# Optimization experiments

Hardware: AMD Instinct MI355X
Metric: run time of the kernel (lower is better)

The kernel has to match this reference:

```python
import jax, jax.numpy as jnp
import numpy as np

KEY_DIM = 64
DENSE_DIM = 128
B, N, M = 8, 2048, 256


def setup_inputs() -> dict:
    key = jax.random.key(0)
    ks = jax.random.split(key, 10)
    s_in = 1.0 / np.sqrt(M)
    s_k = 1.0 / np.sqrt(KEY_DIM)
    s_d = 1.0 / np.sqrt(DENSE_DIM)
    return {
        "x": jax.random.normal(ks[0], (B, N, M), dtype=jnp.float32),
        "Wq": jax.random.normal(ks[1], (M, KEY_DIM), dtype=jnp.float32) * s_in,
        "Wk": jax.random.normal(ks[2], (M, KEY_DIM), dtype=jnp.float32) * s_in,
        "Wv": jax.random.normal(ks[3], (M, KEY_DIM), dtype=jnp.float32) * s_in,
        "W1": jax.random.normal(ks[4], (KEY_DIM, DENSE_DIM), dtype=jnp.float32) * s_k,
        "b1": jnp.zeros((DENSE_DIM,), dtype=jnp.float32),
        "W2": jax.random.normal(ks[5], (DENSE_DIM, DENSE_DIM), dtype=jnp.float32) * s_d,
        "b2": jnp.zeros((DENSE_DIM,), dtype=jnp.float32),
        "W3": jax.random.normal(ks[6], (DENSE_DIM, DENSE_DIM), dtype=jnp.float32) * s_d,
        "b3": jnp.zeros((DENSE_DIM,), dtype=jnp.float32),
    }


def reference(x, Wq, Wk, Wv, W1, b1, W2, b2, W3, b3):
    scale = np.sqrt(KEY_DIM).astype(np.float32)
    q = jnp.einsum('bnm,mk->bnk', x, Wq)
    k = jnp.einsum('bnm,mk->bnk', x, Wk)
    v = jnp.einsum('bnm,mk->bnk', x, Wv)
    scores = jnp.einsum('bik,bjk->bij', q, k) / scale  # [B, N, N]
    weights = jax.nn.softmax(scores, axis=-1)
    z = jnp.einsum('bij,bjk->bik', weights, v)  # [B, N, key_dim]
    h = jax.nn.elu(z @ W1 + b1)
    h = jax.nn.elu(h @ W2 + b2)
    out = jax.nn.elu(h @ W3 + b3)
    return out
```

## Files before the change

kernel.cpp:

```cpp
#include <hip/hip_runtime.h>
#include <cstdint>
#include <cstddef>

#define B_ 8
#define N_ 2048
#define M_ 256
#define KD 64
#define DD 128
#define BN (B_ * N_)
#define KSPLIT 4
#define KT_PER (N_ / 64 / KSPLIT)

typedef __attribute__((ext_vector_type(8))) short s16x8;
typedef __attribute__((ext_vector_type(4))) float f32x4;
typedef __attribute__((ext_vector_type(4))) unsigned int u32x4;

__device__ __forceinline__ float elu_f(float x) {
    return x > 0.f ? x : (__expf(x) - 1.f);
}

__device__ __forceinline__ unsigned short f2bf(float f) {
    unsigned int u = __float_as_uint(f);
    u = (u + 0x7FFFu + ((u >> 16) & 1u)) >> 16;
    return (unsigned short)u;
// ... 51 lines not shown
        int id2 = id - 6144;
        if (id2 < 1024) {
            ct = id2 >> 7; c = (id2 >> 6) & 1; lane = id2 & 63;
            W = W1; ncol = DD; ph = pW1h; pl = pW1l;
            base = ((ct * 2 + c) * 64 + lane) * 8;
        } else if (id2 < 3072) {
            int id3 = id2 - 1024;
            ct = id3 >> 8; c = (id3 >> 6) & 3; lane = id3 & 63;
            W = W2; ncol = DD; ph = pW2h; pl = pW2l;
            base = ((ct * 4 + c) * 64 + lane) * 8;
        } else {
            int id3 = id2 - 3072;
            ct = id3 >> 8; c = (id3 >> 6) & 3; lane = id3 & 63;
            W = W3; ncol = DD; ph = pW3h; pl = pW3l;
            base = ((ct * 4 + c) * 64 + lane) * 8;
        }
    }
    const int col = ct * 16 + (lane & 15);
    const int kb = c * 32 + (lane >> 4) * 8;
    #pragma unroll
    for (int j = 0; j < 8; ++j) {
        float v = W[(size_t)(kb + j) * ncol + col];
        unsigned short h = f2bf(v);
        ph[base + j] = h;
        pl[base + j] = bflo(v, h);
    }
}

__global__ __launch_bounds__(256)
void qkv_kernel(const float* __restrict__ x,
                const unsigned short* __restrict__ pQh,
                unsigned short* __restrict__ qb, unsigned short* __restrict__ kb,
                unsigned short* __restrict__ vtb) {
    __shared__ unsigned short xh[16 * 264];
    __shared__ float dbuf[16 * 204];
    const int t = threadIdx.x;
    const int row0 = blockIdx.x * 16;

    for (int i = t; i < 1024; i += 256) {
        int rr = i >> 6, c4 = i & 63;
        float4 v = reinterpret_cast<const float4*>(x + (size_t)(row0 + rr) * M_)[c4];
        ushort4 o;
        o.x = f2bf(v.x); o.y = f2bf(v.y); o.z = f2bf(v.z); o.w = f2bf(v.w);
        *reinterpret_cast<ushort4*>(&xh[rr * 264 + c4 * 4]) = o;
    }
    __syncthreads();

    const int w = t >> 6, l = t & 63, g = l >> 4, r = l & 15;

    f32x4 acc0 = {0.f, 0.f, 0.f, 0.f};
    f32x4 acc1 = {0.f, 0.f, 0.f, 0.f};
    f32x4 acc2 = {0.f, 0.f, 0.f, 0.f};
    const int t0 = 3 * w, t1 = 3 * w + 1, t2 = 3 * w + 2;

    #pragma unroll
    for (int c = 0; c < 8; ++c) {
        const s16x8 af = *reinterpret_cast<const s16x8*>(&xh[r * 264 + c * 32 + g * 8]);
        const s16x8 b0 = *reinterpret_cast<const s16x8*>(pQh + ((t0 * 8 + c) * 64 + l) * 8);
        const s16x8 b1 = *reinterpret_cast<const s16x8*>(pQh + ((t1 * 8 + c) * 64 + l) * 8);
        const s16x8 b2 = *reinterpret_cast<const s16x8*>(pQh + ((t2 * 8 + c) * 64 + l) * 8);
        acc0 = __builtin_amdgcn_mfma_f32_16x16x32_bf16(af, b0, acc0, 0, 0, 0);
        acc1 = __builtin_amdgcn_mfma_f32_16x16x32_bf16(af, b1, acc1, 0, 0, 0);
        acc2 = __builtin_amdgcn_mfma_f32_16x16x32_bf16(af, b2, acc2, 0, 0, 0);
    }

    {
        const int c0 = (t0 >> 2) * 68 + (t0 & 3) * 16 + r;
        const int c1 = (t1 >> 2) * 68 + (t1 & 3) * 16 + r;
        const int c2 = (t2 >> 2) * 68 + (t2 & 3) * 16 + r;
        #pragma unroll
        for (int reg = 0; reg < 4; ++reg) {
            dbuf[(4 * g + reg) * 204 + c0] = acc0[reg];
            dbuf[(4 * g + reg) * 204 + c1] = acc1[reg];
            dbuf[(4 * g + reg) * 204 + c2] = acc2[reg];
        }
    }
    __syncthreads();

    const int b = row0 >> 11, n0 = row0 & 2047;
    if (t < 128) {
        const int mat = t >> 6, rr = (t >> 2) & 15, cq = t & 3;
        const float* src = &dbuf[rr * 204 + mat * 68 + cq * 16];
        float4 v0 = *reinterpret_cast<const float4*>(src);
        float4 v1 = *reinterpret_cast<const float4*>(src + 4);
        float4 v2 = *reinterpret_cast<const float4*>(src + 8);
        float4 v3 = *reinterpret_cast<const float4*>(src + 12);
        const float sc = (mat == 0) ? 0.125f : 1.0f;
        uint4 o0, o1;
        o0.x = bfpack2(v0.x * sc, v0.y * sc);
        o0.y = bfpack2(v0.z * sc, v0.w * sc);
        o0.z = bfpack2(v1.x * sc, v1.y * sc);
        o0.w = bfpack2(v1.z * sc, v1.w * sc);
        o1.x = bfpack2(v2.x * sc, v2.y * sc);
        o1.y = bfpack2(v2.z * sc, v2.w * sc);
        o1.z = bfpack2(v3.x * sc, v3.y * sc);
        o1.w = bfpack2(v3.z * sc, v3.w * sc);
        unsigned short* dst = (mat == 0 ? qb : kb) + (size_t)(row0 + rr) * KD + cq * 16;
        *reinterpret_cast<uint4*>(dst)     = o0;
        *reinterpret_cast<uint4*>(dst + 8) = o1;
    } else if (t < 192) {
        const int d = t & 63;
        unsigned short tmp[16];
        #pragma unroll
        for (int i = 0; i < 16; ++i)
            tmp[i] = f2bf(dbuf[i * 204 + 136 + d]);
        uint4 o0, o1;
        o0.x = (unsigned)tmp[0]  | ((unsigned)tmp[1]  << 16);
        o0.y = (unsigned)tmp[2]  | ((unsigned)tmp[3]  << 16);
        o0.z = (unsigned)tmp[4]  | ((unsigned)tmp[5]  << 16);
        o0.w = (unsigned)tmp[6]  | ((unsigned)tmp[7]  << 16);
        o1.x = (unsigned)tmp[8]  | ((unsigned)tmp[9]  << 16);
        o1.y = (unsigned)tmp[10] | ((unsigned)tmp[11] << 16);
        o1.z = (unsigned)tmp[12] | ((unsigned)tmp[13] << 16);
        o1.w = (unsigned)tmp[14] | ((unsigned)tmp[15] << 16);
        unsigned short* vp = vtb + ((size_t)b * KD + d) * N_ + n0;
        *reinterpret_cast<uint4*>(vp)     = o0;
        *reinterpret_cast<uint4*>(vp + 8) = o1;
    }
}

__global__ __launch_bounds__(256)
void attn_kernel(const unsigned short* __restrict__ qb,
                 const unsigned short* __restrict__ kb,
                 const unsigned short* __restrict__ vtb,
                 float* __restrict__ Zp, float* __restrict__ lsum) {
    __shared__ __align__(16) unsigned short ks[64 * 72];
    __shared__ __align__(16) unsigned short vt[64 * 72];
    __shared__ __align__(16) unsigned short ps[4 * 16 * 72];

    const int t = threadIdx.x;
    const int w = t >> 6;
    const int l = t & 63;
    const int g = l >> 4;
    const int r = l & 15;
    const int bid = blockIdx.x;
    const int split = bid & 3;
    const int qt = (bid >> 2) & 31;
    const int bb = bid >> 7;
    const int qrow0 = qt * 64 + w * 16;
    const int k0 = split * (N_ / KSPLIT);

    const unsigned short* qrow = qb + ((size_t)bb * N_ + qrow0 + r) * KD + g * 8;
    const s16x8 qf0 = *reinterpret_cast<const s16x8*>(qrow);
    const s16x8 qf1 = *reinterpret_cast<const s16x8*>(qrow + 32);

    const unsigned short* kbase = kb + ((size_t)bb * N_ + k0) * KD;
    const unsigned short* vbase = vtb + (size_t)bb * KD * N_ + k0;
    unsigned short* psw = ps + w * (16 * 72);

    for (int c = t; c < 512; c += 256) {
        int key = c >> 3, sub = c & 7;
        *reinterpret_cast<s16x8*>(&ks[key * 72 + sub * 8]) =
            *reinterpret_cast<const s16x8*>(kbase + (size_t)key * KD + sub * 8);
        *reinterpret_cast<s16x8*>(&vt[key * 72 + sub * 8]) =
            *reinterpret_cast<const s16x8*>(vbase + (size_t)key * N_ + sub * 8);
    }
    __syncthreads();

    f32x4 zac0 = {0.f, 0.f, 0.f, 0.f};
    f32x4 zac1 = {0.f, 0.f, 0.f, 0.f};
    f32x4 zac2 = {0.f, 0.f, 0.f, 0.f};
    f32x4 zac3 = {0.f, 0.f, 0.f, 0.f};
    float lacc[4] = {0.f, 0.f, 0.f, 0.f};

    const int ck0 = (t >> 3), cs0 = (t & 7);
    const int ck1 = ((t + 256) >> 3), cs1 = ((t + 256) & 7);

    for (int kt = 0; kt < KT_PER; ++kt) {
        s16x8 kr0, kr1, vr0, vr1;
        const bool pf = (kt + 1 < KT_PER);
        if (pf) {
            const unsigned short* kg = kbase + (size_t)(kt + 1) * 64 * KD;
            const unsigned short* vg = vbase + (size_t)(kt + 1) * 64;
            kr0 = *reinterpret_cast<const s16x8*>(kg + (size_t)ck0 * KD + cs0 * 8);
            kr1 = *reinterpret_cast<const s16x8*>(kg + (size_t)ck1 * KD + cs1 * 8);
            vr0 = *reinterpret_cast<const s16x8*>(vg + (size_t)ck0 * N_ + cs0 * 8);
            vr1 = *reinterpret_cast<const s16x8*>(vg + (size_t)ck1 * N_ + cs1 * 8);
        }

        f32x4 s0 = {0.f, 0.f, 0.f, 0.f};
        f32x4 s1 = {0.f, 0.f, 0.f, 0.f};
        f32x4 s2 = {0.f, 0.f, 0.f, 0.f};
        f32x4 s3 = {0.f, 0.f, 0.f, 0.f};
        {
            const s16x8 kf00 = *reinterpret_cast<const s16x8*>(&ks[(r +  0) * 72 + g * 8]);
            const s16x8 kf01 = *reinterpret_cast<const s16x8*>(&ks[(r +  0) * 72 + g * 8 + 32]);
            const s16x8 kf10 = *reinterpret_cast<const s16x8*>(&ks[(r + 16) * 72 + g * 8]);
            const s16x8 kf11 = *reinterpret_cast<const s16x8*>(&ks[(r + 16) * 72 + g * 8 + 32]);
            const s16x8 kf20 = *reinterpret_cast<const s16x8*>(&ks[(r + 32) * 72 + g * 8]);
            const s16x8 kf21 = *reinterpret_cast<const s16x8*>(&ks[(r + 32) * 72 + g * 8 + 32]);
            const s16x8 kf30 = *reinterpret_cast<const s16x8*>(&ks[(r + 48) * 72 + g * 8]);
            const s16x8 kf31 = *reinterpret_cast<const s16x8*>(&ks[(r + 48) * 72 + g * 8 + 32]);
            s0 = __builtin_amdgcn_mfma_f32_16x16x32_bf16(qf0, kf00, s0, 0, 0, 0);
            s0 = __builtin_amdgcn_mfma_f32_16x16x32_bf16(qf1, kf01, s0, 0, 0, 0);
            s1 = __builtin_amdgcn_mfma_f32_16x16x32_bf16(qf0, kf10, s1, 0, 0, 0);
            s1 = __builtin_amdgcn_mfma_f32_16x16x32_bf16(qf1, kf11, s1, 0, 0, 0);
            s2 = __builtin_amdgcn_mfma_f32_16x16x32_bf16(qf0, kf20, s2, 0, 0, 0);
            s2 = __builtin_amdgcn_mfma_f32_16x16x32_bf16(qf1, kf21, s2, 0, 0, 0);
            s3 = __builtin_amdgcn_mfma_f32_16x16x32_bf16(qf0, kf30, s3, 0, 0, 0);
            s3 = __builtin_amdgcn_mfma_f32_16x16x32_bf16(qf1, kf31, s3, 0, 0, 0);
        }

        const s16x8 vf00 = *reinterpret_cast<const s16x8*>(&vt[(r +  0) * 72 + g * 8]);
        const s16x8 vf01 = *reinterpret_cast<const s16x8*>(&vt[(r +  0) * 72 + g * 8 + 32]);
        const s16x8 vf10 = *reinterpret_cast<const s16x8*>(&vt[(r + 16) * 72 + g * 8]);
        const s16x8 vf11 = *reinterpret_cast<const s16x8*>(&vt[(r + 16) * 72 + g * 8 + 32]);
        const s16x8 vf20 = *reinterpret_cast<const s16x8*>(&vt[(r + 32) * 72 + g * 8]);
        const s16x8 vf21 = *reinterpret_cast<const s16x8*>(&vt[(r + 32) * 72 + g * 8 + 32]);
        const s16x8 vf30 = *reinterpret_cast<const s16x8*>(&vt[(r + 48) * 72 + g * 8]);
        const s16x8 vf31 = *reinterpret_cast<const s16x8*>(&vt[(r + 48) * 72 + g * 8 + 32]);

        #pragma unroll
        for (int j = 0; j < 4; ++j) {
            float p0 = __expf(s0[j]);
            float p1 = __expf(s1[j]);
            float p2 = __expf(s2[j]);
            float p3 = __expf(s3[j]);
            lacc[j] += (p0 + p1) + (p2 + p3);
            psw[(4 * g + j) * 72 + r +  0] = f2bf(p0);
            psw[(4 * g + j) * 72 + r + 16] = f2bf(p1);
            psw[(4 * g + j) * 72 + r + 32] = f2bf(p2);
            psw[(4 * g + j) * 72 + r + 48] = f2bf(p3);
        }

        asm volatile("s_waitcnt lgkmcnt(0)" ::: "memory");
        __builtin_amdgcn_sched_barrier(0);

        const s16x8 pa0 = *reinterpret_cast<const s16x8*>(&psw[r * 72 + g * 8]);
        const s16x8 pa1 = *reinterpret_cast<const s16x8*>(&psw[r * 72 + g * 8 + 32]);
        zac0 = __builtin_amdgcn_mfma_f32_16x16x32_bf16(pa0, vf00, zac0, 0, 0, 0);
        zac0 = __builtin_amdgcn_mfma_f32_16x16x32_bf16(pa1, vf01, zac0, 0, 0, 0);
        zac1 = __builtin_amdgcn_mfma_f32_16x16x32_bf16(pa0, vf10, zac1, 0, 0, 0);
        zac1 = __builtin_amdgcn_mfma_f32_16x16x32_bf16(pa1, vf11, zac1, 0, 0, 0);
        zac2 = __builtin_amdgcn_mfma_f32_16x16x32_bf16(pa0, vf20, zac2, 0, 0, 0);
        zac2 = __builtin_amdgcn_mfma_f32_16x16x32_bf16(pa1, vf21, zac2, 0, 0, 0);
        zac3 = __builtin_amdgcn_mfma_f32_16x16x32_bf16(pa0, vf30, zac3, 0, 0, 0);
        zac3 = __builtin_amdgcn_mfma_f32_16x16x32_bf16(pa1, vf31, zac3, 0, 0, 0);

        __syncthreads();
        if (pf) {
            *reinterpret_cast<s16x8*>(&ks[ck0 * 72 + cs0 * 8]) = kr0;
            *reinterpret_cast<s16x8*>(&ks[ck1 * 72 + cs1 * 8]) = kr1;
            *reinterpret_cast<s16x8*>(&vt[ck0 * 72 + cs0 * 8]) = vr0;
            *reinterpret_cast<s16x8*>(&vt[ck1 * 72 + cs1 * 8]) = vr1;
        }
        __syncthreads();
    }

    const size_t rowbase = (size_t)split * BN + (size_t)bb * N_ + qrow0;
    #pragma unroll
    for (int j = 0; j < 4; ++j) {
        float lt = lacc[j];
        lt += __shfl_xor(lt, 1);
        lt += __shfl_xor(lt, 2);
        lt += __shfl_xor(lt, 4);
        lt += __shfl_xor(lt, 8);
        if (r == 0)
            lsum[rowbase + 4 * g + j] = lt;
        float* zr = Zp + (rowbase + 4 * g + j) * KD + r;
        zr[ 0] = zac0[j];
        zr[16] = zac1[j];
        zr[32] = zac2[j];
        zr[48] = zac3[j];
    }
}

__global__ __launch_bounds__(256)
void mlp_kernel(const float* __restrict__ Zp, const float* __restrict__ lsum,
                const unsigned short* __restrict__ pW1h, const unsigned short* __restrict__ pW1l,
                const unsigned short* __restrict__ pW2h, const unsigned short* __restrict__ pW2l,
                const unsigned short* __restrict__ pW3h, const unsigned short* __restrict__ pW3l,
                const float* __restrict__ b1, const float* __restrict__ b2,
                const float* __restrict__ b3, float* __restrict__ out) {
    __shared__ unsigned int zW[16 * 68];
    __shared__ unsigned int hW[16 * 140];
    const int t = threadIdx.x;
    const int row0 = blockIdx.x * 16;

    {
        const int rr = t >> 4, dq = (t & 15) * 4;
        const size_t grow = (size_t)row0 + rr;
        const float inv = 1.0f / (lsum[grow] + lsum[BN + grow] +
                                  lsum[2 * (size_t)BN + grow] + lsum[3 * (size_t)BN + grow]);
        const size_t off = grow * KD + dq;
        float4 v0 = *reinterpret_cast<const float4*>(Zp + off);
        float4 v1 = *reinterpret_cast<const float4*>(Zp + (size_t)BN * KD + off);
        float4 v2 = *reinterpret_cast<const float4*>(Zp + 2 * (size_t)BN * KD + off);
        float4 v3 = *reinterpret_cast<const float4*>(Zp + 3 * (size_t)BN * KD + off);
        uint4 wv;
        wv.x = packw((v0.x + v1.x + v2.x + v3.x) * inv);
        wv.y = packw((v0.y + v1.y + v2.y + v3.y) * inv);
        wv.z = packw((v0.z + v1.z + v2.z + v3.z) * inv);
        wv.w = packw((v0.w + v1.w + v2.w + v3.w) * inv);
        *reinterpret_cast<uint4*>(&zW[rr * 68 + dq]) = wv;
    }
    __syncthreads();

    const int w = t >> 6, l = t & 63, g = l >> 4, r = l & 15;
    const int ctA = 2 * w, ctB = 2 * w + 1;

    f32x4 a1A = {0.f, 0.f, 0.f, 0.f};
    f32x4 a1B = {0.f, 0.f, 0.f, 0.f};
    #pragma unroll
    for (int c = 0; c < 2; ++c) {
        s16x8 ahi, alo;
        unpack8(&zW[r * 68 + c * 32 + g * 8], ahi, alo);
        const int baseA = ((ctA * 2 + c) * 64 + l) * 8;
        const int baseB = ((ctB * 2 + c) * 64 + l) * 8;
        const s16x8 bhA = *reinterpret_cast<const s16x8*>(pW1h + baseA);
        const s16x8 blA = *reinterpret_cast<const s16x8*>(pW1l + baseA);
        const s16x8 bhB = *reinterpret_cast<const s16x8*>(pW1h + baseB);
        const s16x8 blB = *reinterpret_cast<const s16x8*>(pW1l + baseB);
        a1A = __builtin_amdgcn_mfma_f32_16x16x32_bf16(ahi, bhA, a1A, 0, 0, 0);
        a1A = __builtin_amdgcn_mfma_f32_16x16x32_bf16(ahi, blA, a1A, 0, 0, 0);
        a1A = __builtin_amdgcn_mfma_f32_16x16x32_bf16(alo, bhA, a1A, 0, 0, 0);
        a1B = __builtin_amdgcn_mfma_f32_16x16x32_bf16(ahi, bhB, a1B, 0, 0, 0);
        a1B = __builtin_amdgcn_mfma_f32_16x16x32_bf16(ahi, blB, a1B, 0, 0, 0);
        a1B = __builtin_amdgcn_mfma_f32_16x16x32_bf16(alo, bhB, a1B, 0, 0, 0);
    }
    {
        const float bvA = b1[ctA * 16 + r], bvB = b1[ctB * 16 + r];
        #pragma unroll
        for (int reg = 0; reg < 4; ++reg) {
            hW[(4 * g + reg) * 140 + ctA * 16 + r] = packw(elu_f(a1A[reg] + bvA));
            hW[(4 * g + reg) * 140 + ctB * 16 + r] = packw(elu_f(a1B[reg] + bvB));
        }
    }
    __syncthreads();

    f32x4 a2A = {0.f, 0.f, 0.f, 0.f};
    f32x4 a2B = {0.f, 0.f, 0.f, 0.f};
    #pragma unroll
    for (int c = 0; c < 4; ++c) {
        s16x8 ahi, alo;
        unpack8(&hW[r * 140 + c * 32 + g * 8], ahi, alo);
        const int baseA = ((ctA * 4 + c) * 64 + l) * 8;
        const int baseB = ((ctB * 4 + c) * 64 + l) * 8;
        const s16x8 bhA = *reinterpret_cast<const s16x8*>(pW2h + baseA);
        const s16x8 blA = *reinterpret_cast<const s16x8*>(pW2l + baseA);
        const s16x8 bhB = *reinterpret_cast<const s16x8*>(pW2h + baseB);
        const s16x8 blB = *reinterpret_cast<const s16x8*>(pW2l + baseB);
        a2A = __builtin_amdgcn_mfma_f32_16x16x32_bf16(ahi, bhA, a2A, 0, 0, 0);
        a2A = __builtin_amdgcn_mfma_f32_16x16x32_bf16(ahi, blA, a2A, 0, 0, 0);
        a2A = __builtin_amdgcn_mfma_f32_16x16x32_bf16(alo, bhA, a2A, 0, 0, 0);
        a2B = __builtin_amdgcn_mfma_f32_16x16x32_bf16(ahi, bhB, a2B, 0, 0, 0);
        a2B = __builtin_amdgcn_mfma_f32_16x16x32_bf16(ahi, blB, a2B, 0, 0, 0);
        a2B = __builtin_amdgcn_mfma_f32_16x16x32_bf16(alo, bhB, a2B, 0, 0, 0);
    }
    __syncthreads();
    {
        const float bvA = b2[ctA * 16 + r], bvB = b2[ctB * 16 + r];
        #pragma unroll
        for (int reg = 0; reg < 4; ++reg) {
            hW[(4 * g + reg) * 140 + ctA * 16 + r] = packw(elu_f(a2A[reg] + bvA));
            hW[(4 * g + reg) * 140 + ctB * 16 + r] = packw(elu_f(a2B[reg] + bvB));
        }
    }
    __syncthreads();

    f32x4 a3A = {0.f, 0.f, 0.f, 0.f};
    f32x4 a3B = {0.f, 0.f, 0.f, 0.f};
    #pragma unroll
    for (int c = 0; c < 4; ++c) {
        s16x8 ahi, alo;
        unpack8(&hW[r * 140 + c * 32 + g * 8], ahi, alo);
        const int baseA = ((ctA * 4 + c) * 64 + l) * 8;
        const int baseB = ((ctB * 4 + c) * 64 + l) * 8;
        const s16x8 bhA = *reinterpret_cast<const s16x8*>(pW3h + baseA);
        const s16x8 blA = *reinterpret_cast<const s16x8*>(pW3l + baseA);
        const s16x8 bhB = *reinterpret_cast<const s16x8*>(pW3h + baseB);
        const s16x8 blB = *reinterpret_cast<const s16x8*>(pW3l + baseB);
        a3A = __builtin_amdgcn_mfma_f32_16x16x32_bf16(ahi, bhA, a3A, 0, 0, 0);
        a3A = __builtin_amdgcn_mfma_f32_16x16x32_bf16(ahi, blA, a3A, 0, 0, 0);
        a3A = __builtin_amdgcn_mfma_f32_16x16x32_bf16(alo, bhA, a3A, 0, 0, 0);
        a3B = __builtin_amdgcn_mfma_f32_16x16x32_bf16(ahi, bhB, a3B, 0, 0, 0);
        a3B = __builtin_amdgcn_mfma_f32_16x16x32_bf16(ahi, blB, a3B, 0, 0, 0);
        a3B = __builtin_amdgcn_mfma_f32_16x16x32_bf16(alo, bhB, a3B, 0, 0, 0);
    }
    {
        const float bvA = b3[ctA * 16 + r], bvB = b3[ctB * 16 + r];
        #pragma unroll
        for (int reg = 0; reg < 4; ++reg) {
            float* orow = out + (size_t)(row0 + 4 * g + reg) * DD;
            orow[ctA * 16 + r] = elu_f(a3A[reg] + bvA);
            orow[ctB * 16 + r] = elu_f(a3B[reg] + bvB);
        }
    }
}

extern "C" void kernel_launch(void* const* d_in, const int* in_sizes, int n_in,
                              void* d_out, int out_size, void* d_ws, size_t ws_size,
                              hipStream_t stream) {
    (void)in_sizes; (void)n_in; (void)out_size; (void)ws_size;
    const float* x  = (const float*)d_in[0];
    const float* Wq = (const float*)d_in[1];
    const float* Wk = (const float*)d_in[2];
    const float* Wv = (const float*)d_in[3];
    const float* W1 = (const float*)d_in[4];
    const float* b1 = (const float*)d_in[5];
    const float* W2 = (const float*)d_in[6];
    const float* b2 = (const float*)d_in[7];
    const float* W3 = (const float*)d_in[8];
    const float* b3 = (const float*)d_in[9];
    float* out = (float*)d_out;

    const size_t nt = (size_t)BN * KD;
    unsigned short* qbf = (unsigned short*)d_ws;
    unsigned short* kbf = qbf + nt;
    unsigned short* vtb = kbf + nt;
    float* Zp   = (float*)(vtb + nt);
    float* lsum = Zp + (size_t)KSPLIT * nt;
    unsigned short* pQh  = (unsigned short*)(lsum + (size_t)KSPLIT * BN);
    unsigned short* pQl  = pQh + 49152;
    unsigned short* pW1h = pQl + 49152;
    unsigned short* pW1l = pW1h + 8192;
    unsigned short* pW2h = pW1l + 8192;
    unsigned short* pW2l = pW2h + 16384;
    unsigned short* pW3h = pW2l + 16384;
    unsigned short* pW3l = pW3h + 16384;

    pack_kernel<<<dim3(44), 256, 0, stream>>>(Wq, Wk, Wv, W1, W2, W3,
                                              pQh, pQl, pW1h, pW1l, pW2h, pW2l, pW3h, pW3l);
    qkv_kernel<<<dim3(BN / 16), 256, 0, stream>>>(x, pQh, qbf, kbf, vtb);
    attn_kernel<<<dim3(BN / 64 * KSPLIT), 256, 0, stream>>>(qbf, kbf, vtb, Zp, lsum);
    mlp_kernel<<<dim3(BN / 16), 256, 0, stream>>>(Zp, lsum, pW1h, pW1l, pW2h, pW2l,
                                                  pW3h, pW3l, b1, b2, b3, out);
}
```

Baseline: 54.80 us.

## Give each wave two 16-row tiles in qkv, attention and MLP kernels

Each wave now handles 32 rows instead of 16 in all three main kernels. The qkv and MLP kernels process 32 rows per block, and attention uses 2 waves of 128 threads per block, each covering 32 query rows. The aim is to reuse the loaded B fragments (weights, K and V tiles) across two MFMA row tiles, halving fragment loads per flop and cutting global/LDS traffic per output. The cost is more registers per wave, fewer waves per block in attention, and half as many blocks in qkv and MLP, which lowers occupancy and parallelism.

```diff
diff --git a/kernel.cpp b/kernel.cpp
--- a/kernel.cpp
+++ b/kernel.cpp
@@ -107,12 +107,12 @@
                 const unsigned short* __restrict__ pQh,
                 unsigned short* __restrict__ qb, unsigned short* __restrict__ kb,
                 unsigned short* __restrict__ vtb) {
-    __shared__ unsigned short xh[16 * 264];
-    __shared__ float dbuf[16 * 204];
+    __shared__ unsigned short xh[32 * 264];
+    __shared__ float dbuf[32 * 204];
     const int t = threadIdx.x;
-    const int row0 = blockIdx.x * 16;
-
-    for (int i = t; i < 1024; i += 256) {
+    const int row0 = blockIdx.x * 32;
+
+    for (int i = t; i < 2048; i += 256) {
         int rr = i >> 6, c4 = i & 63;
         float4 v = reinterpret_cast<const float4*>(x + (size_t)(row0 + rr) * M_)[c4];
         ushort4 o;
@@ -122,21 +122,28 @@
     __syncthreads();
 
     const int w = t >> 6, l = t & 63, g = l >> 4, r = l & 15;
-
-    f32x4 acc0 = {0.f, 0.f, 0.f, 0.f};
-    f32x4 acc1 = {0.f, 0.f, 0.f, 0.f};
-    f32x4 acc2 = {0.f, 0.f, 0.f, 0.f};
     const int t0 = 3 * w, t1 = 3 * w + 1, t2 = 3 * w + 2;
 
+    f32x4 acc[3][2];
+    #pragma unroll
+    for (int m = 0; m < 3; ++m)
+        #pragma unroll
+        for (int s = 0; s < 2; ++s)
+            acc[m][s] = (f32x4){0.f, 0.f, 0.f, 0.f};
+
     #pragma unroll
     for (int c = 0; c < 8; ++c) {
-        const s16x8 af = *reinterpret_cast<const s16x8*>(&xh[r * 264 + c * 32 + g * 8]);
+        const s16x8 a0 = *reinterpret_cast<const s16x8*>(&xh[r * 264 + c * 32 + g * 8]);
+        const s16x8 a1 = *reinterpret_cast<const s16x8*>(&xh[(16 + r) * 264 + c * 32 + g * 8]);
         const s16x8 b0 = *reinterpret_cast<const s16x8*>(pQh + ((t0 * 8 + c) * 64 + l) * 8);
         const s16x8 b1 = *reinterpret_cast<const s16x8*>(pQh + ((t1 * 8 + c) * 64 + l) * 8);
         const s16x8 b2 = *reinterpret_cast<const s16x8*>(pQh + ((t2 * 8 + c) * 64 + l) * 8);
-        acc0 = __builtin_amdgcn_mfma_f32_16x16x32_bf16(af, b0, acc0, 0, 0, 0);
-        acc1 = __builtin_amdgcn_mfma_f32_16x16x32_bf16(af, b1, acc1, 0, 0, 0);
-        acc2 = __builtin_amdgcn_mfma_f32_16x16x32_bf16(af, b2, acc2, 0, 0, 0);
+        acc[0][0] = __builtin_amdgcn_mfma_f32_16x16x32_bf16(a0, b0, acc[0][0], 0, 0, 0);
+        acc[0][1] = __builtin_amdgcn_mfma_f32_16x16x32_bf16(a1, b0, acc[0][1], 0, 0, 0);
+        acc[1][0] = __builtin_amdgcn_mfma_f32_16x16x32_bf16(a0, b1, acc[1][0], 0, 0, 0);
+        acc[1][1] = __builtin_amdgcn_mfma_f32_16x16x32_bf16(a1, b1, acc[1][1], 0, 0, 0);
+        acc[2][0] = __builtin_amdgcn_mfma_f32_16x16x32_bf16(a0, b2, acc[2][0], 0, 0, 0);
+        acc[2][1] = __builtin_amdgcn_mfma_f32_16x16x32_bf16(a1, b2, acc[2][1], 0, 0, 0);
     }
 
     {
@@ -144,17 +151,20 @@
         const int c1 = (t1 >> 2) * 68 + (t1 & 3) * 16 + r;
         const int c2 = (t2 >> 2) * 68 + (t2 & 3) * 16 + r;
         #pragma unroll
-        for (int reg = 0; reg < 4; ++reg) {
-            dbuf[(4 * g + reg) * 204 + c0] = acc0[reg];
-            dbuf[(4 * g + reg) * 204 + c1] = acc1[reg];
-            dbuf[(4 * g + reg) * 204 + c2] = acc2[reg];
-        }
+        for (int s = 0; s < 2; ++s)
+            #pragma unroll
+            for (int reg = 0; reg < 4; ++reg) {
+                const int rw = (s * 16 + 4 * g + reg) * 204;
+                dbuf[rw + c0] = acc[0][s][reg];
+                dbuf[rw + c1] = acc[1][s][reg];
+                dbuf[rw + c2] = acc[2][s][reg];
+            }
     }
     __syncthreads();
 
     const int b = row0 >> 11, n0 = row0 & 2047;
-    if (t < 128) {
-        const int mat = t >> 6, rr = (t >> 2) & 15, cq = t & 3;
+    {
+        const int mat = t >> 7, rem = t & 127, rr = rem >> 2, cq = rem & 3;
         const float* src = &dbuf[rr * 204 + mat * 68 + cq * 16];
         float4 v0 = *reinterpret_cast<const float4*>(src);
         float4 v1 = *reinterpret_cast<const float4*>(src + 4);
@@ -173,35 +183,30 @@
         unsigned short* dst = (mat == 0 ? qb : kb) + (size_t)(row0 + rr) * KD + cq * 16;
         *reinterpret_cast<uint4*>(dst)     = o0;
         *reinterpret_cast<uint4*>(dst + 8) = o1;
-    } else if (t < 192) {
-        const int d = t & 63;
-        unsigned short tmp[16];
-        #pragma unroll
-        for (int i = 0; i < 16; ++i)
-            tmp[i] = f2bf(dbuf[i * 204 + 136 + d]);
-        uint4 o0, o1;
-        o0.x = (unsigned)tmp[0]  | ((unsigned)tmp[1]  << 16);
-        o0.y = (unsigned)tmp[2]  | ((unsigned)tmp[3]  << 16);
-        o0.z = (unsigned)tmp[4]  | ((unsigned)tmp[5]  << 16);
-        o0.w = (unsigned)tmp[6]  | ((unsigned)tmp[7]  << 16);
-        o1.x = (unsigned)tmp[8]  | ((unsigned)tmp[9]  << 16);
-        o1.y = (unsigned)tmp[10] | ((unsigned)tmp[11] << 16);
-        o1.z = (unsigned)tmp[12] | ((unsigned)tmp[13] << 16);
-        o1.w = (unsigned)tmp[14] | ((unsigned)tmp[15] << 16);
-        unsigned short* vp = vtb + ((size_t)b * KD + d) * N_ + n0;
-        *reinterpret_cast<uint4*>(vp)     = o0;
-        *reinterpret_cast<uint4*>(vp + 8) = o1;
-    }
-}
-
-__global__ __launch_bounds__(256)
+    }
+    {
+        const int d = t >> 2, ng = (t & 3) * 8;
+        unsigned short tmp[8];
+        #pragma unroll
+        for (int i = 0; i < 8; ++i)
+            tmp[i] = f2bf(dbuf[(ng + i) * 204 + 136 + d]);
+        uint4 o0;
+        o0.x = (unsigned)tmp[0] | ((unsigned)tmp[1] << 16);
+        o0.y = (unsigned)tmp[2] | ((unsigned)tmp[3] << 16);
+        o0.z = (unsigned)tmp[4] | ((unsigned)tmp[5] << 16);
+        o0.w = (unsigned)tmp[6] | ((unsigned)tmp[7] << 16);
+        *reinterpret_cast<uint4*>(vtb + ((size_t)b * KD + d) * N_ + n0 + ng) = o0;
+    }
+}
+
+__global__ __launch_bounds__(128)
 void attn_kernel(const unsigned short* __restrict__ qb,
                  const unsigned short* __restrict__ kb,
                  const unsigned short* __restrict__ vtb,
                  float* __restrict__ Zp, float* __restrict__ lsum) {
     __shared__ __align__(16) unsigned short ks[64 * 72];
     __shared__ __align__(16) unsigned short vt[64 * 72];
-    __shared__ __align__(16) unsigned short ps[4 * 16 * 72];
+    __shared__ __align__(16) unsigned short ps[2 * 32 * 72];
 
     const int t = threadIdx.x;
     const int w = t >> 6;
@@ -212,18 +217,21 @@
     const int split = bid & 3;
     const int qt = (bid >> 2) & 31;
     const int bb = bid >> 7;
-    const int qrow0 = qt * 64 + w * 16;
+    const int qrow0 = qt * 64 + w * 32;
     const int k0 = split * (N_ / KSPLIT);
 
-    const unsigned short* qrow = qb + ((size_t)bb * N_ + qrow0 + r) * KD + g * 8;
-    const s16x8 qf0 = *reinterpret_cast<const s16x8*>(qrow);
-    const s16x8 qf1 = *reinterpret_cast<const s16x8*>(qrow + 32);
+    const unsigned short* qrowA = qb + ((size_t)bb * N_ + qrow0 + r) * KD + g * 8;
+    const unsigned short* qrowB = qrowA + (size_t)16 * KD;
+    const s16x8 qfA0 = *reinterpret_cast<const s16x8*>(qrowA);
+    const s16x8 qfA1 = *reinterpret_cast<const s16x8*>(qrowA + 32);
+    const s16x8 qfB0 = *reinterpret_cast<const s16x8*>(qrowB);
+    const s16x8 qfB1 = *reinterpret_cast<const s16x8*>(qrowB + 32);
 
     const unsigned short* kbase = kb + ((size_t)bb * N_ + k0) * KD;
     const unsigned short* vbase = vtb + (size_t)bb * KD * N_ + k0;
-    unsigned short* psw = ps + w * (16 * 72);
-
-    for (int c = t; c < 512; c += 256) {
+    unsigned short* psw = ps + w * (32 * 72);
+
+    for (int c = t; c < 512; c += 128) {
         int key = c >> 3, sub = c & 7;
         *reinterpret_cast<s16x8*>(&ks[key * 72 + sub * 8]) =
             *reinterpret_cast<const s16x8*>(kbase + (size_t)key * KD + sub * 8);
@@ -232,31 +240,31 @@
     }
     __syncthreads();
 
-    f32x4 zac0 = {0.f, 0.f, 0.f, 0.f};
-    f32x4 zac1 = {0.f, 0.f, 0.f, 0.f};
-    f32x4 zac2 = {0.f, 0.f, 0.f, 0.f};
-    f32x4 zac3 = {0.f, 0.f, 0.f, 0.f};
-    float lacc[4] = {0.f, 0.f, 0.f, 0.f};
-
-    const int ck0 = (t >> 3), cs0 = (t & 7);
-    const int ck1 = ((t + 256) >> 3), cs1 = ((t + 256) & 7);
+    f32x4 zacA0 = {0.f,0.f,0.f,0.f}, zacA1 = {0.f,0.f,0.f,0.f};
+    f32x4 zacA2 = {0.f,0.f,0.f,0.f}, zacA3 = {0.f,0.f,0.f,0.f};
+    f32x4 zacB0 = {0.f,0.f,0.f,0.f}, zacB1 = {0.f,0.f,0.f,0.f};
+    f32x4 zacB2 = {0.f,0.f,0.f,0.f}, zacB3 = {0.f,0.f,0.f,0.f};
+    float laccA[4] = {0.f, 0.f, 0.f, 0.f};
+    float laccB[4] = {0.f, 0.f, 0.f, 0.f};
 
     for (int kt = 0; kt < KT_PER; ++kt) {
-        s16x8 kr0, kr1, vr0, vr1;
+        s16x8 kr[4], vr[4];
         const bool pf = (kt + 1 < KT_PER);
         if (pf) {
             const unsigned short* kg = kbase + (size_t)(kt + 1) * 64 * KD;
             const unsigned short* vg = vbase + (size_t)(kt + 1) * 64;
-            kr0 = *reinterpret_cast<const s16x8*>(kg + (size_t)ck0 * KD + cs0 * 8);
-            kr1 = *reinterpret_cast<const s16x8*>(kg + (size_t)ck1 * KD + cs1 * 8);
-            vr0 = *reinterpret_cast<const s16x8*>(vg + (size_t)ck0 * N_ + cs0 * 8);
-            vr1 = *reinterpret_cast<const s16x8*>(vg + (size_t)ck1 * N_ + cs1 * 8);
-        }
-
-        f32x4 s0 = {0.f, 0.f, 0.f, 0.f};
-        f32x4 s1 = {0.f, 0.f, 0.f, 0.f};
-        f32x4 s2 = {0.f, 0.f, 0.f, 0.f};
-        f32x4 s3 = {0.f, 0.f, 0.f, 0.f};
+            #pragma unroll
+            for (int i = 0; i < 4; ++i) {
+                const int c = t + 128 * i, key = c >> 3, sub = c & 7;
+                kr[i] = *reinterpret_cast<const s16x8*>(kg + (size_t)key * KD + sub * 8);
+                vr[i] = *reinterpret_cast<const s16x8*>(vg + (size_t)key * N_ + sub * 8);
+            }
+        }
+
+        f32x4 sA0 = {0.f,0.f,0.f,0.f}, sA1 = {0.f,0.f,0.f,0.f};
+        f32x4 sA2 = {0.f,0.f,0.f,0.f}, sA3 = {0.f,0.f,0.f,0.f};
+        f32x4 sB0 = {0.f,0.f,0.f,0.f}, sB1 = {0.f,0.f,0.f,0.f};
+        f32x4 sB2 = {0.f,0.f,0.f,0.f}, sB3 = {0.f,0.f,0.f,0.f};
         {
             const s16x8 kf00 = *reinterpret_cast<const s16x8*>(&ks[(r +  0) * 72 + g * 8]);
             const s16x8 kf01 = *reinterpret_cast<const s16x8*>(&ks[(r +  0) * 72 + g * 8 + 32]);
@@ -266,14 +274,22 @@
             const s16x8 kf21 = *reinterpret_cast<const s16x8*>(&ks[(r + 32) * 72 + g * 8 + 32]);
             const s16x8 kf30 = *reinterpret_cast<const s16x8*>(&ks[(r + 48) * 72 + g * 8]);
             const s16x8 kf31 = *reinterpret_cast<const s16x8*>(&ks[(r + 48) * 72 + g * 8 + 32]);
-            s0 = __builtin_amdgcn_mfma_f32_16x16x32_bf16(qf0, kf00, s0, 0, 0, 0);
-            s0 = __builtin_amdgcn_mfma_f32_16x16x32_bf16(qf1, kf01, s0, 0, 0, 0);
-            s1 = __builtin_amdgcn_mfma_f32_16x16x32_bf16(qf0, kf10, s1, 0, 0, 0);
-            s1 = __builtin_amdgcn_mfma_f32_16x16x32_bf16(qf1, kf11, s1, 0, 0, 0);
-            s2 = __builtin_amdgcn_mfma_f32_16x16x32_bf16(qf0, kf20, s2, 0, 0, 0);
-            s2 = __builtin_amdgcn_mfma_f32_16x16x32_bf16(qf1, kf21, s2, 0, 0, 0);
-            s3 = __builtin_amdgcn_mfma_f32_16x16x32_bf16(qf0, kf30, s3, 0, 0, 0);
-            s3 = __builtin_amdgcn_mfma_f32_16x16x32_bf16(qf1, kf31, s3, 0, 0, 0);
+            sA0 = __builtin_amdgcn_mfma_f32_16x16x32_bf16(qfA0, kf00, sA0, 0, 0, 0);
+            sA0 = __builtin_amdgcn_mfma_f32_16x16x32_bf16(qfA1, kf01, sA0, 0, 0, 0);
+            sA1 = __builtin_amdgcn_mfma_f32_16x16x32_bf16(qfA0, kf10, sA1, 0, 0, 0);
+            sA1 = __builtin_amdgcn_mfma_f32_16x16x32_bf16(qfA1, kf11, sA1, 0, 0, 0);
+            sA2 = __builtin_amdgcn_mfma_f32_16x16x32_bf16(qfA0, kf20, sA2, 0, 0, 0);
+            sA2 = __builtin_amdgcn_mfma_f32_16x16x32_bf16(qfA1, kf21, sA2, 0, 0, 0);
+            sA3 = __builtin_amdgcn_mfma_f32_16x16x32_bf16(qfA0, kf30, sA3, 0, 0, 0);
+            sA3 = __builtin_amdgcn_mfma_f32_16x16x32_bf16(qfA1, kf31, sA3, 0, 0, 0);
+            sB0 = __builtin_amdgcn_mfma_f32_16x16x32_bf16(qfB0, kf00, sB0, 0, 0, 0);
+            sB0 = __builtin_amdgcn_mfma_f32_16x16x32_bf16(qfB1, kf01, sB0, 0, 0, 0);
+            sB1 = __builtin_amdgcn_mfma_f32_16x16x32_bf16(qfB0, kf10, sB1, 0, 0, 0);
+            sB1 = __builtin_amdgcn_mfma_f32_16x16x32_bf16(qfB1, kf11, sB1, 0, 0, 0);
+            sB2 = __builtin_amdgcn_mfma_f32_16x16x32_bf16(qfB0, kf20, sB2, 0, 0, 0);
+            sB2 = __builtin_amdgcn_mfma_f32_16x16x32_bf16(qfB1, kf21, sB2, 0, 0, 0);
+            sB3 = __builtin_amdgcn_mfma_f32_16x16x32_bf16(qfB0, kf30, sB3, 0, 0, 0);
+            sB3 = __builtin_amdgcn_mfma_f32_16x16x32_bf16(qfB1, kf31, sB3, 0, 0, 0);
         }
 
         const s16x8 vf00 = *reinterpret_cast<const s16x8*>(&vt[(r +  0) * 72 + g * 8]);
@@ -287,37 +303,61 @@
 
         #pragma unroll
         for (int j = 0; j < 4; ++j) {
-            float p0 = __expf(s0[j]);
-            float p1 = __expf(s1[j]);
-            float p2 = __expf(s2[j]);
-            float p3 = __expf(s3[j]);
-            lacc[j] += (p0 + p1) + (p2 + p3);
+            float p0 = __expf(sA0[j]);
+            float p1 = __expf(sA1[j]);
+            float p2 = __expf(sA2[j]);
+            float p3 = __expf(sA3[j]);
+            laccA[j] += (p0 + p1) + (p2 + p3);
             psw[(4 * g + j) * 72 + r +  0] = f2bf(p0);
             psw[(4 * g + j) * 72 + r + 16] = f2bf(p1);
             psw[(4 * g + j) * 72 + r + 32] = f2bf(p2);
             psw[(4 * g + j) * 72 + r + 48] = f2bf(p3);
         }
+        #pragma unroll
+        for (int j = 0; j < 4; ++j) {
+            float p0 = __expf(sB0[j]);
+            float p1 = __expf(sB1[j]);
+            float p2 = __expf(sB2[j]);
+            float p3 = __expf(sB3[j]);
+            laccB[j] += (p0 + p1) + (p2 + p3);
+            psw[(16 + 4 * g + j) * 72 + r +  0] = f2bf(p0);
+            psw[(16 + 4 * g + j) * 72 + r + 16] = f2bf(p1);
+            psw[(16 + 4 * g + j) * 72 + r + 32] = f2bf(p2);
+            psw[(16 + 4 * g + j) * 72 + r + 48] = f2bf(p3);
+        }
 
         asm volatile("s_waitcnt lgkmcnt(0)" ::: "memory");
         __builtin_amdgcn_sched_barrier(0);
 
-        const s16x8 pa0 = *reinterpret_cast<const s16x8*>(&psw[r * 72 + g * 8]);
-        const s16x8 pa1 = *reinterpret_cast<const s16x8*>(&psw[r * 72 + g * 8 + 32]);
-        zac0 = __builtin_amdgcn_mfma_f32_16x16x32_bf16(pa0, vf00, zac0, 0, 0, 0);
-        zac0 = __builtin_amdgcn_mfma_f32_16x16x32_bf16(pa1, vf01, zac0, 0, 0, 0);
-        zac1 = __builtin_amdgcn_mfma_f32_16x16x32_bf16(pa0, vf10, zac1, 0, 0, 0);
-        zac1 = __builtin_amdgcn_mfma_f32_16x16x32_bf16(pa1, vf11, zac1, 0, 0, 0);
-        zac2 = __builtin_amdgcn_mfma_f32_16x16x32_bf16(pa0, vf20, zac2, 0, 0, 0);
-        zac2 = __builtin_amdgcn_mfma_f32_16x16x32_bf16(pa1, vf21, zac2, 0, 0, 0);
-        zac3 = __builtin_amdgcn_mfma_f32_16x16x32_bf16(pa0, vf30, zac3, 0, 0, 0);
-        zac3 = __builtin_amdgcn_mfma_f32_16x16x32_bf16(pa1, vf31, zac3, 0, 0, 0);
+        const s16x8 paA0 = *reinterpret_cast<const s16x8*>(&psw[r * 72 + g * 8]);
+        const s16x8 paA1 = *reinterpret_cast<const s16x8*>(&psw[r * 72 + g * 8 + 32]);
+        const s16x8 paB0 = *reinterpret_cast<const s16x8*>(&psw[(16 + r) * 72 + g * 8]);
+        const s16x8 paB1 = *reinterpret_cast<const s16x8*>(&psw[(16 + r) * 72 + g * 8 + 32]);
+        zacA0 = __builtin_amdgcn_mfma_f32_16x16x32_bf16(paA0, vf00, zacA0, 0, 0, 0);
+        zacA0 = __builtin_amdgcn_mfma_f32_16x16x32_bf16(paA1, vf01, zacA0, 0, 0, 0);
+        zacA1 = __builtin_amdgcn_mfma_f32_16x16x32_bf16(paA0, vf10, zacA1, 0, 0, 0);
+        zacA1 = __builtin_amdgcn_mfma_f32_16x16x32_bf16(paA1, vf11, zacA1, 0, 0, 0);
+        zacA2 = __builtin_amdgcn_mfma_f32_16x16x32_bf16(paA0, vf20, zacA2, 0, 0, 0);
+        zacA2 = __builtin_amdgcn_mfma_f32_16x16x32_bf16(paA1, vf21, zacA2, 0, 0, 0);
+        zacA3 = __builtin_amdgcn_mfma_f32_16x16x32_bf16(paA0, vf30, zacA3, 0, 0, 0);
+        zacA3 = __builtin_amdgcn_mfma_f32_16x16x32_bf16(paA1, vf31, zacA3, 0, 0, 0);
+        zacB0 = __builtin_amdgcn_mfma_f32_16x16x32_bf16(paB0, vf00, zacB0, 0, 0, 0);
+        zacB0 = __builtin_amdgcn_mfma_f32_16x16x32_bf16(paB1, vf01, zacB0, 0, 0, 0);
+        zacB1 = __builtin_amdgcn_mfma_f32_16x16x32_bf16(paB0, vf10, zacB1, 0, 0, 0);
+        zacB1 = __builtin_amdgcn_mfma_f32_16x16x32_bf16(paB1, vf11, zacB1, 0, 0, 0);
+        zacB2 = __builtin_amdgcn_mfma_f32_16x16x32_bf16(paB0, vf20, zacB2, 0, 0, 0);
+        zacB2 = __builtin_amdgcn_mfma_f32_16x16x32_bf16(paB1, vf21, zacB2, 0, 0, 0);
+        zacB3 = __builtin_amdgcn_mfma_f32_16x16x32_bf16(paB0, vf30, zacB3, 0, 0, 0);
+        zacB3 = __builtin_amdgcn_mfma_f32_16x16x32_bf16(paB1, vf31, zacB3, 0, 0, 0);
 
         __syncthreads();
         if (pf) {
-            *reinterpret_cast<s16x8*>(&ks[ck0 * 72 + cs0 * 8]) = kr0;
-            *reinterpret_cast<s16x8*>(&ks[ck1 * 72 + cs1 * 8]) = kr1;
-            *reinterpret_cast<s16x8*>(&vt[ck0 * 72 + cs0 * 8]) = vr0;
-            *reinterpret_cast<s16x8*>(&vt[ck1 * 72 + cs1 * 8]) = vr1;
+            #pragma unroll
+            for (int i = 0; i < 4; ++i) {
+                const int c = t + 128 * i, key = c >> 3, sub = c & 7;
+                *reinterpret_cast<s16x8*>(&ks[key * 72 + sub * 8]) = kr[i];
+                *reinterpret_cast<s16x8*>(&vt[key * 72 + sub * 8]) = vr[i];
+            }
         }
         __syncthreads();
     }
@@ -325,7 +365,7 @@
     const size_t rowbase = (size_t)split * BN + (size_t)bb * N_ + qrow0;
     #pragma unroll
     for (int j = 0; j < 4; ++j) {
-        float lt = lacc[j];
+        float lt = laccA[j];
         lt += __shfl_xor(lt, 1);
         lt += __shfl_xor(lt, 2);
         lt += __shfl_xor(lt, 4);
@@ -333,10 +373,25 @@
         if (r == 0)
             lsum[rowbase + 4 * g + j] = lt;
         float* zr = Zp + (rowbase + 4 * g + j) * KD + r;
-        zr[ 0] = zac0[j];
-        zr[16] = zac1[j];
-        zr[32] = zac2[j];
-        zr[48] = zac3[j];
+        zr[ 0] = zacA0[j];
+        zr[16] = zacA1[j];
+        zr[32] = zacA2[j];
+        zr[48] = zacA3[j];
+    }
+    #pragma unroll
+    for (int j = 0; j < 4; ++j) {
+        float lt = laccB[j];
+        lt += __shfl_xor(lt, 1);
+        lt += __shfl_xor(lt, 2);
+        lt += __shfl_xor(lt, 4);
+        lt += __shfl_xor(lt, 8);
+        if (r == 0)
+            lsum[rowbase + 16 + 4 * g + j] = lt;
+        float* zr = Zp + (rowbase + 16 + 4 * g + j) * KD + r;
+        zr[ 0] = zacB0[j];
+        zr[16] = zacB1[j];
+        zr[32] = zacB2[j];
+        zr[48] = zacB3[j];
     }
 }
 
@@ -347,119 +402,162 @@
                 const unsigned short* __restrict__ pW3h, const unsigned short* __restrict__ pW3l,
                 const float* __restrict__ b1, const float* __restrict__ b2,
                 const float* __restrict__ b3, float* __restrict__ out) {
-    __shared__ unsigned int zW[16 * 68];
-    __shared__ unsigned int hW[16 * 140];
+    __shared__ unsigned int zW[32 * 68];
+    __shared__ unsigned int hW[32 * 140];
     const int t = threadIdx.x;
-    const int row0 = blockIdx.x * 16;
+    const int row0 = blockIdx.x * 32;
 
     {
-        const int rr = t >> 4, dq = (t & 15) * 4;
+        const int rr = t >> 3, c8 = (t & 7) * 8;
         const size_t grow = (size_t)row0 + rr;
         const float inv = 1.0f / (lsum[grow] + lsum[BN + grow] +
                                   lsum[2 * (size_t)BN + grow] + lsum[3 * (size_t)BN + grow]);
-        const size_t off = grow * KD + dq;
-        float4 v0 = *reinterpret_cast<const float4*>(Zp + off);
-        float4 v1 = *reinterpret_cast<const float4*>(Zp + (size_t)BN * KD + off);
-        float4 v2 = *reinterpret_cast<const float4*>(Zp + 2 * (size_t)BN * KD + off);
-        float4 v3 = *reinterpret_cast<const float4*>(Zp + 3 * (size_t)BN * KD + off);
-        uint4 wv;
-        wv.x = packw((v0.x + v1.x + v2.x + v3.x) * inv);
-        wv.y = packw((v0.y + v1.y + v2.y + v3.y) * inv);
-        wv.z = packw((v0.z + v1.z + v2.z + v3.z) * inv);
-        wv.w = packw((v0.w + v1.w + v2.w + v3.w) * inv);
-        *reinterpret_cast<uint4*>(&zW[rr * 68 + dq]) = wv;
+        const size_t off = grow * KD + c8;
+        uint4 wv0, wv1;
+        {
+            float4 a0 = *reinterpret_cast<const float4*>(Zp + off);
+            float4 a1 = *reinterpret_cast<const float4*>(Zp + (size_t)BN * KD + off);
+            float4 a2 = *reinterpret_cast<const float4*>(Zp + 2 * (size_t)BN * KD + off);
+            float4 a3 = *reinterpret_cast<const float4*>(Zp + 3 * (size_t)BN * KD + off);
+            wv0.x = packw((a0.x + a1.x + a2.x + a3.x) * inv);
+            wv0.y = packw((a0.y + a1.y + a2.y + a3.y) * inv);
+            wv0.z = packw((a0.z + a1.z + a2.z + a3.z) * inv);
+            wv0.w = packw((a0.w + a1.w + a2.w + a3.w) * inv);
+        }
+        {
+            float4 a0 = *reinterpret_cast<const float4*>(Zp + off + 4);
+            float4 a1 = *reinterpret_cast<const float4*>(Zp + (size_t)BN * KD + off + 4);
+            float4 a2 = *reinterpret_cast<const float4*>(Zp + 2 * (size_t)BN * KD + off + 4);
+            float4 a3 = *reinterpret_cast<const float4*>(Zp + 3 * (size_t)BN * KD + off + 4);
+            wv1.x = packw((a0.x + a1.x + a2.x + a3.x) * inv);
+            wv1.y = packw((a0.y + a1.y + a2.y + a3.y) * inv);
+            wv1.z = packw((a0.z + a1.z + a2.z + a3.z) * inv);
+            wv1.w = packw((a0.w + a1.w + a2.w + a3.w) * inv);
+        }
+        *reinterpret_cast<uint4*>(&zW[rr * 68 + c8])     = wv0;
+        *reinterpret_cast<uint4*>(&zW[rr * 68 + c8 + 4]) = wv1;
     }
     __syncthreads();
 
     const int w = t >> 6, l = t & 63, g = l >> 4, r = l & 15;
     const int ctA = 2 * w, ctB = 2 * w + 1;
 
-    f32x4 a1A = {0.f, 0.f, 0.f, 0.f};
-    f32x4 a1B = {0.f, 0.f, 0.f, 0.f};
+    f32x4 aA[2], aB[2];
+    #pragma unroll
+    for (int s = 0; s < 2; ++s) { aA[s] = (f32x4){0,0,0,0}; aB[s] = (f32x4){0,0,0,0}; }
     #pragma unroll
     for (int c = 0; c < 2; ++c) {
-        s16x8 ahi, alo;
-        unpack8(&zW[r * 68 + c * 32 + g * 8], ahi, alo);
+        s16x8 h0, l0, h1, l1;
+        unpack8(&zW[r * 68 + c * 32 + g * 8], h0, l0);
+        unpack8(&zW[(16 + r) * 68 + c * 32 + g * 8], h1, l1);
         const int baseA = ((ctA * 2 + c) * 64 + l) * 8;
         const int baseB = ((ctB * 2 + c) * 64 + l) * 8;
         const s16x8 bhA = *reinterpret_cast<const s16x8*>(pW1h + baseA);
         const s16x8 blA = *reinterpret_cast<const s16x8*>(pW1l + baseA);
         const s16x8 bhB = *reinterpret_cast<const s16x8*>(pW1h + baseB);
         const s16x8 blB = *reinterpret_cast<const s16x8*>(pW1l + baseB);
-        a1A = __builtin_amdgcn_mfma_f32_16x16x32_bf16(ahi, bhA, a1A, 0, 0, 0);
-        a1A = __builtin_amdgcn_mfma_f32_16x16x32_bf16(ahi, blA, a1A, 0, 0, 0);
-        a1A = __builtin_amdgcn_mfma_f32_16x16x32_bf16(alo, bhA, a1A, 0, 0, 0);
-        a1B = __builtin_amdgcn_mfma_f32_16x16x32_bf16(ahi, bhB, a1B, 0, 0, 0);
-        a1B = __builtin_amdgcn_mfma_f32_16x16x32_bf16(ahi, blB, a1B, 0, 0, 0);
-        a1B = __builtin_amdgcn_mfma_f32_16x16x32_bf16(alo, bhB, a1B, 0, 0, 0);
+        aA[0] = __builtin_amdgcn_mfma_f32_16x16x32_bf16(h0, bhA, aA[0], 0, 0, 0);
+        aA[0] = __builtin_amdgcn_mfma_f32_16x16x32_bf16(h0, blA, aA[0], 0, 0, 0);
+        aA[0] = __builtin_amdgcn_mfma_f32_16x16x32_bf16(l0, bhA, aA[0], 0, 0, 0);
+        aA[1] = __builtin_amdgcn_mfma_f32_16x16x32_bf16(h1, bhA, aA[1], 0, 0, 0);
+        aA[1] = __builtin_amdgcn_mfma_f32_16x16x32_bf16(h1, blA, aA[1], 0, 0, 0);
+        aA[1] = __builtin_amdgcn_mfma_f32_16x16x32_bf16(l1, bhA, aA[1], 0, 0, 0);
+        aB[0] = __builtin_amdgcn_mfma_f32_16x16x32_bf16(h0, bhB, aB[0], 0, 0, 0);
+        aB[0] = __builtin_amdgcn_mfma_f32_16x16x32_bf16(h0, blB, aB[0], 0, 0, 0);
+        aB[0] = __builtin_amdgcn_mfma_f32_16x16x32_bf16(l0, bhB, aB[0], 0, 0, 0);
+        aB[1] = __builtin_amdgcn_mfma_f32_16x16x32_bf16(h1, bhB, aB[1], 0, 0, 0);
+        aB[1] = __builtin_amdgcn_mfma_f32_16x16x32_bf16(h1, blB, aB[1], 0, 0, 0);
+        aB[1] = __builtin_amdgcn_mfma_f32_16x16x32_bf16(l1, bhB, aB[1], 0, 0, 0);
     }
     {
         const float bvA = b1[ctA * 16 + r], bvB = b1[ctB * 16 + r];
         #pragma unroll
-        for (int reg = 0; reg < 4; ++reg) {
-            hW[(4 * g + reg) * 140 + ctA * 16 + r] = packw(elu_f(a1A[reg] + bvA));
-            hW[(4 * g + reg) * 140 + ctB * 16 + r] = packw(elu_f(a1B[reg] + bvB));
-        }
+        for (int s = 0; s < 2; ++s)
+            #pragma unroll
+            for (int reg = 0; reg < 4; ++reg) {
+                const int rw = (s * 16 + 4 * g + reg) * 140;
+                hW[rw + ctA * 16 + r] = packw(elu_f(aA[s][reg] + bvA));
+                hW[rw + ctB * 16 + r] = packw(elu_f(aB[s][reg] + bvB));
+            }
     }
     __syncthreads();
 
-    f32x4 a2A = {0.f, 0.f, 0.f, 0.f};
-    f32x4 a2B = {0.f, 0.f, 0.f, 0.f};
+    #pragma unroll
+    for (int s = 0; s < 2; ++s) { aA[s] = (f32x4){0,0,0,0}; aB[s] = (f32x4){0,0,0,0}; }
     #pragma unroll
     for (int c = 0; c < 4; ++c) {
-        s16x8 ahi, alo;
-        unpack8(&hW[r * 140 + c * 32 + g * 8], ahi, alo);
+        s16x8 h0, l0, h1, l1;
+        unpack8(&hW[r * 140 + c * 32 + g * 8], h0, l0);
+        unpack8(&hW[(16 + r) * 140 + c * 32 + g * 8], h1, l1);
         const int baseA = ((ctA * 4 + c) * 64 + l) * 8;
         const int baseB = ((ctB * 4 + c) * 64 + l) * 8;
         const s16x8 bhA = *reinterpret_cast<const s16x8*>(pW2h + baseA);
         const s16x8 blA = *reinterpret_cast<const s16x8*>(pW2l + baseA);
         const s16x8 bhB = *reinterpret_cast<const s16x8*>(pW2h + baseB);
         const s16x8 blB = *reinterpret_cast<const s16x8*>(pW2l + baseB);
-        a2A = __builtin_amdgcn_mfma_f32_16x16x32_bf16(ahi, bhA, a2A, 0, 0, 0);
-        a2A = __builtin_amdgcn_mfma_f32_16x16x32_bf16(ahi, blA, a2A, 0, 0, 0);
-        a2A = __builtin_amdgcn_mfma_f32_16x16x32_bf16(alo, bhA, a2A, 0, 0, 0);
-        a2B = __builtin_amdgcn_mfma_f32_16x16x32_bf16(ahi, bhB, a2B, 0, 0, 0);
-        a2B = __builtin_amdgcn_mfma_f32_16x16x32_bf16(ahi, blB, a2B, 0, 0, 0);
-        a2B = __builtin_amdgcn_mfma_f32_16x16x32_bf16(alo, bhB, a2B, 0, 0, 0);
+        aA[0] = __builtin_amdgcn_mfma_f32_16x16x32_bf16(h0, bhA, aA[0], 0, 0, 0);
+        aA[0] = __builtin_amdgcn_mfma_f32_16x16x32_bf16(h0, blA, aA[0], 0, 0, 0);
+        aA[0] = __builtin_amdgcn_mfma_f32_16x16x32_bf16(l0, bhA, aA[0], 0, 0, 0);
+        aA[1] = __builtin_amdgcn_mfma_f32_16x16x32_bf16(h1, bhA, aA[1], 0, 0, 0);
+        aA[1] = __builtin_amdgcn_mfma_f32_16x16x32_bf16(h1, blA, aA[1], 0, 0, 0);
+        aA[1] = __builtin_amdgcn_mfma_f32_16x16x32_bf16(l1, bhA, aA[1], 0, 0, 0);
+        aB[0] = __builtin_amdgcn_mfma_f32_16x16x32_bf16(h0, bhB, aB[0], 0, 0, 0);
+        aB[0] = __builtin_amdgcn_mfma_f32_16x16x32_bf16(h0, blB, aB[0], 0, 0, 0);
+        aB[0] = __builtin_amdgcn_mfma_f32_16x16x32_bf16(l0, bhB, aB[0], 0, 0, 0);
+        aB[1] = __builtin_amdgcn_mfma_f32_16x16x32_bf16(h1, bhB, aB[1], 0, 0, 0);
+        aB[1] = __builtin_amdgcn_mfma_f32_16x16x32_bf16(h1, blB, aB[1], 0, 0, 0);
+        aB[1] = __builtin_amdgcn_mfma_f32_16x16x32_bf16(l1, bhB, aB[1], 0, 0, 0);
     }
     __syncthreads();
     {
         const float bvA = b2[ctA * 16 + r], bvB = b2[ctB * 16 + r];
         #pragma unroll
-        for (int reg = 0; reg < 4; ++reg) {
-            hW[(4 * g + reg) * 140 + ctA * 16 + r] = packw(elu_f(a2A[reg] + bvA));
-            hW[(4 * g + reg) * 140 + ctB * 16 + r] = packw(elu_f(a2B[reg] + bvB));
-        }
+        for (int s = 0; s < 2; ++s)
+            #pragma unroll
+            for (int reg = 0; reg < 4; ++reg) {
+                const int rw = (s * 16 + 4 * g + reg) * 140;
+                hW[rw + ctA * 16 + r] = packw(elu_f(aA[s][reg] + bvA));
+                hW[rw + ctB * 16 + r] = packw(elu_f(aB[s][reg] + bvB));
+            }
     }
     __syncthreads();
 
-    f32x4 a3A = {0.f, 0.f, 0.f, 0.f};
-    f32x4 a3B = {0.f, 0.f, 0.f, 0.f};
+    #pragma unroll
+    for (int s = 0; s < 2; ++s) { aA[s] = (f32x4){0,0,0,0}; aB[s] = (f32x4){0,0,0,0}; }
     #pragma unroll
     for (int c = 0; c < 4; ++c) {
-        s16x8 ahi, alo;
-        unpack8(&hW[r * 140 + c * 32 + g * 8], ahi, alo);
+        s16x8 h0, l0, h1, l1;
+        unpack8(&hW[r * 140 + c * 32 + g * 8], h0, l0);
+        unpack8(&hW[(16 + r) * 140 + c * 32 + g * 8], h1, l1);
         const int baseA = ((ctA * 4 + c) * 64 + l) * 8;
         const int baseB = ((ctB * 4 + c) * 64 + l) * 8;
         const s16x8 bhA = *reinterpret_cast<const s16x8*>(pW3h + baseA);
         const s16x8 blA = *reinterpret_cast<const s16x8*>(pW3l + baseA);
         const s16x8 bhB = *reinterpret_cast<const s16x8*>(pW3h + baseB);
         const s16x8 blB = *reinterpret_cast<const s16x8*>(pW3l + baseB);
-        a3A = __builtin_amdgcn_mfma_f32_16x16x32_bf16(ahi, bhA, a3A, 0, 0, 0);
-        a3A = __builtin_amdgcn_mfma_f32_16x16x32_bf16(ahi, blA, a3A, 0, 0, 0);
-        a3A = __builtin_amdgcn_mfma_f32_16x16x32_bf16(alo, bhA, a3A, 0, 0, 0);
-        a3B = __builtin_amdgcn_mfma_f32_16x16x32_bf16(ahi, bhB, a3B, 0, 0, 0);
-        a3B = __builtin_amdgcn_mfma_f32_16x16x32_bf16(ahi, blB, a3B, 0, 0, 0);
-        a3B = __builtin_amdgcn_mfma_f32_16x16x32_bf16(alo, bhB, a3B, 0, 0, 0);
+        aA[0] = __builtin_amdgcn_mfma_f32_16x16x32_bf16(h0, bhA, aA[0], 0, 0, 0);
+        aA[0] = __builtin_amdgcn_mfma_f32_16x16x32_bf16(h0, blA, aA[0], 0, 0, 0);
+        aA[0] = __builtin_amdgcn_mfma_f32_16x16x32_bf16(l0, bhA, aA[0], 0, 0, 0);
+        aA[1] = __builtin_amdgcn_mfma_f32_16x16x32_bf16(h1, bhA, aA[1], 0, 0, 0);
+        aA[1] = __builtin_amdgcn_mfma_f32_16x16x32_bf16(h1, blA, aA[1], 0, 0, 0);
+        aA[1] = __builtin_amdgcn_mfma_f32_16x16x32_bf16(l1, bhA, aA[1], 0, 0, 0);
+        aB[0] = __builtin_amdgcn_mfma_f32_16x16x32_bf16(h0, bhB, aB[0], 0, 0, 0);
+        aB[0] = __builtin_amdgcn_mfma_f32_16x16x32_bf16(h0, blB, aB[0], 0, 0, 0);
+        aB[0] = __builtin_amdgcn_mfma_f32_16x16x32_bf16(l0, bhB, aB[0], 0, 0, 0);
+        aB[1] = __builtin_amdgcn_mfma_f32_16x16x32_bf16(h1, bhB, aB[1], 0, 0, 0);
+        aB[1] = __builtin_amdgcn_mfma_f32_16x16x32_bf16(h1, blB, aB[1], 0, 0, 0);
+        aB[1] = __builtin_amdgcn_mfma_f32_16x16x32_bf16(l1, bhB, aB[1], 0, 0, 0);
     }
     {
         const float bvA = b3[ctA * 16 + r], bvB = b3[ctB * 16 + r];
         #pragma unroll
-        for (int reg = 0; reg < 4; ++reg) {
-            float* orow = out + (size_t)(row0 + 4 * g + reg) * DD;
-            orow[ctA * 16 + r] = elu_f(a3A[reg] + bvA);
-            orow[ctB * 16 + r] = elu_f(a3B[reg] + bvB);
-        }
+        for (int s = 0; s < 2; ++s)
+            #pragma unroll
+            for (int reg = 0; reg < 4; ++reg) {
+                float* orow = out + (size_t)(row0 + s * 16 + 4 * g + reg) * DD;
+                orow[ctA * 16 + r] = elu_f(aA[s][reg] + bvA);
+                orow[ctB * 16 + r] = elu_f(aB[s][reg] + bvB);
+            }
     }
 }
 
@@ -496,8 +594,8 @@
 
     pack_kernel<<<dim3(44), 256, 0, stream>>>(Wq, Wk, Wv, W1, W2, W3,
                                               pQh, pQl, pW1h, pW1l, pW2h, pW2l, pW3h, pW3l);
-    qkv_kernel<<<dim3(BN / 16), 256, 0, stream>>>(x, pQh, qbf, kbf, vtb);
-    attn_kernel<<<dim3(BN / 64 * KSPLIT), 256, 0, stream>>>(qbf, kbf, vtb, Zp, lsum);
-    mlp_kernel<<<dim3(BN / 16), 256, 0, stream>>>(Zp, lsum, pW1h, pW1l, pW2h, pW2l,
+    qkv_kernel<<<dim3(BN / 32), 256, 0, stream>>>(x, pQh, qbf, kbf, vtb);
+    attn_kernel<<<dim3(BN / 64 * KSPLIT), 128, 0, stream>>>(qbf, kbf, vtb, Zp, lsum);
+    mlp_kernel<<<dim3(BN / 32), 256, 0, stream>>>(Zp, lsum, pW1h, pW1l, pW2h, pW2l,
                                                   pW3h, pW3l, b1, b2, b3, out);
 }
```

Result: no change. 55.02 us (+0.4%).
